# Performance work log

Hardware: AMD Instinct MI355X
Metric: run time of the kernel (lower is better)

Reference implementation:

```python
import jax, jax.numpy as jnp
import numpy as np
from jax import lax

BITS = 8  # w_p = a_p = 8 (HAWQ int8)

def _round_ste(x):
    # straight-through round (quant-aware training semantics)
    return x + lax.stop_gradient(jnp.round(x) - x)

def _quant_act(x):
    # QuantAct: symmetric per-tensor activation fake-quant; returns (quantized x, scale)
    n = 2.0 ** (BITS - 1) - 1.0
    sf = jnp.maximum(jnp.max(jnp.abs(x)) / n, 1e-8)
    q = jnp.clip(_round_ste(x / sf), -n, n)
    return q * sf, sf

def _quant_conv(x, w, b, pre_sf, stride, pad):
    # QuantConv2d: per-output-channel symmetric weight quant, integer conv on
    # x/pre_sf with rounded weights, rescale by pre_sf * w_sf. Bias quantized at
    # combined scale. Returns (float output, w_sf) for scale propagation.
    n = 2.0 ** (BITS - 1) - 1.0
    w_sf = jnp.maximum(jnp.max(jnp.abs(w), axis=(1, 2, 3)) / n, 1e-8)
    w_int = _round_ste(w / w_sf[:, None, None, None])
    b_sf = w_sf * pre_sf
    b_int = _round_ste(b / b_sf)
    y = lax.conv_general_dilated(x / pre_sf, w_int, (stride, stride),
                                 [(pad, pad), (pad, pad)],
                                 dimension_numbers=('NCHW', 'OIHW', 'NCHW'))
    return (y + b_int[None, :, None, None]) * b_sf[None, :, None, None], w_sf

def _bn(x, g, b, m, v, eps=1e-5):
    # BatchNorm2d in eval mode (running stats), folded into scale/shift
    inv = g / jnp.sqrt(v + eps)
    return x * inv[None, :, None, None] + (b - m * inv)[None, :, None, None]

def _quant_linear(x, w, b, pre_sf):
    # QuantLinear: per-output-row symmetric weight quant
    n = 2.0 ** (BITS - 1) - 1.0
    w_sf = jnp.maximum(jnp.max(jnp.abs(w), axis=1) / n, 1e-8)
    w_int = _round_ste(w / w_sf[:, None])
    b_sf = w_sf * pre_sf
    b_int = _round_ste(b / b_sf)
    return ((x / pre_sf) @ w_int.T + b_int[None, :]) * b_sf[None, :]

def _forward(x, w0, b0, g0, bb0, m0, v0, w1, b1, g1, bb1, m1, v1,
             w2, b2, g2, bb2, m2, v2, w3, b3, g3, bb3, m3, v3,
             w4, b4, g4, bb4, m4, v4, wd, bd):
    x, psf = _quant_act(x)
    x, _ = _quant_conv(x, w0, b0, psf, 1, 1)   # [B,32,32,32]
    x = _bn(x, g0, bb0, m0, v0)
    x, psf = _quant_act(x)
    x, _ = _quant_conv(x, w1, b1, psf, 1, 0)   # 1x1 -> [B,4,32,32]
    x = _bn(x, g1, bb1, m1, v1)
    x, psf = _quant_act(x)
    x, _ = _quant_conv(x, w2, b2, psf, 2, 1)   # [B,32,16,16]
    x = _bn(x, g2, bb2, m2, v2)
    x, psf = _quant_act(x)
    x, _ = _quant_conv(x, w3, b3, psf, 2, 1)   # [B,32,8,8]
    x = _bn(x, g3, bb3, m3, v3)
    x, psf = _quant_act(x)
    x, _ = _quant_conv(x, w4, b4, psf, 1, 1)   # [B,32,8,8]
    x = _bn(x, g4, bb4, m4, v4)
    x, psf = _quant_act(x)
    x = x.reshape(-1, 2048)                    # 32*8*8 = 2048
    x = _quant_linear(x, wd, bd, psf)          # [B,10]
    return jax.nn.softmax(x, axis=0)           # dim=0 as in original module

def setup_inputs() -> dict:
    key = jax.random.key(0)
    ks = jax.random.split(key, 40)
    B = 1024
    inp = {"x": jax.random.normal(ks[0], (B, 3, 32, 32), jnp.float32)}
    conv_shapes = [(32, 3, 3, 3), (4, 32, 1, 1), (32, 4, 3, 3), (32, 32, 3, 3), (32, 32, 3, 3)]
    for i, s in enumerate(conv_shapes):
        c = s[0]
        inp[f"w{i}"] = jax.random.normal(ks[1 + i], s, jnp.float32) * 0.1
        inp[f"b{i}"] = jax.random.normal(ks[6 + i], (c,), jnp.float32) * 0.01
        inp[f"g{i}"] = 1.0 + 0.1 * jax.random.normal(ks[11 + i], (c,), jnp.float32)
        inp[f"bb{i}"] = 0.1 * jax.random.normal(ks[16 + i], (c,), jnp.float32)
        inp[f"m{i}"] = 0.1 * jax.random.normal(ks[21 + i], (c,), jnp.float32)
        inp[f"v{i}"] = 0.5 + jax.random.uniform(ks[26 + i], (c,), jnp.float32)
    inp["wd"] = jax.random.normal(ks[31], (10, 2048), jnp.float32) * 0.05
    inp["bd"] = jnp.zeros((10,), jnp.float32)
    return inp

def reference(x, w0, b0, g0, bb0, m0, v0, w1, b1, g1, bb1, m1, v1,
              w2, b2, g2, bb2, m2, v2, w3, b3, g3, bb3, m3, v3,
              w4, b4, g4, bb4, m4, v4, wd, bd):
    return _forward(x, w0, b0, g0, bb0, m0, v0, w1, b1, g1, bb1, m1, v1,
                    w2, b2, g2, bb2, m2, v2, w3, b3, g3, bb3, m3, v3,
                    w4, b4, g4, bb4, m4, v4, wd, bd)
```

## Files before the change

### kernel.cpp

```cpp
#include <hip/hip_runtime.h>

#define DI __device__ __forceinline__

constexpr int OFF_WSF0 = 384;
constexpr int OFF_BNS0 = 416;
constexpr int OFF_BNB0 = 448;
constexpr int OFF_W0I  = 480;
constexpr int OFF_WSF1 = 1344;
constexpr int OFF_BNS1 = 1348;
constexpr int OFF_BNB1 = 1352;
constexpr int OFF_W1I  = 1356;
constexpr int OFF_WSF2 = 1484;
constexpr int OFF_BNS2 = 1516;
constexpr int OFF_BNB2 = 1548;
constexpr int OFF_W2I  = 1580;
constexpr int OFF_WSF3 = 2732;
constexpr int OFF_BNS3 = 2764;
constexpr int OFF_BNB3 = 2796;
constexpr int OFF_W3I  = 2828;
constexpr int OFF_WSF4 = 12044;
constexpr int OFF_BNS4 = 12076;
constexpr int OFF_BNB4 = 12108;
constexpr int OFF_W4I  = 12140;
constexpr int OFF_WSFD = 21356;
constexpr int OFF_WDI  = 21368;
constexpr int OFF_LOG  = 41856;
constexpr int OFF_ACT  = 52224;
constexpr long ACT_A_OFF = OFF_ACT;
constexpr long ACT_B_OFF = OFF_ACT + 8388608L;

DI float quantv(float x, float sf) {
    float q = rintf(x / sf);
    return fminf(fmaxf(q, -127.0f), 127.0f);
}
DI float get_sf(const unsigned* umax, int slot) {
    const unsigned* p = umax + slot * 64;
    unsigned m = 0u;
    #pragma unroll
    for (int i = 0; i < 64; ++i) m = m > p[i] ? m : p[i];
    return fmaxf(__uint_as_float(m) / 127.0f, 1e-8f);
}
DI void block_max_atomic(float v, unsigned* dst) {
    __shared__ float redm_[4];
    #pragma unroll
    for (int o = 32; o; o >>= 1) v = fmaxf(v, __shfl_down(v, o, 64));
    int wid = threadIdx.x >> 6;
    if ((threadIdx.x & 63) == 0) redm_[wid] = v;
    __syncthreads();
    if (threadIdx.x == 0) {
        int nw = blockDim.x >> 6;
        float m = redm_[0];
        for (int i = 1; i < nw; ++i) m = fmaxf(m, redm_[i]);
        atomicMax(dst + (blockIdx.x & 63), __float_as_uint(m));
    }
}

struct PrepEntry {
    const float *w, *g, *bb, *m, *v;
    float *wsf, *wint, *bns, *bnb;
    int K; int has_bn;
};
struct PrepAll { PrepEntry e[6]; unsigned* umax; };

__global__ __launch_bounds__(256) void k_prep_all(PrepAll pa) {
    int blk = blockIdx.x;
    if (blk == 142) {
        for (int i = threadIdx.x; i < 384; i += 256) pa.umax[i] = 0u;
        return;
    }
    int layer, oc;
    if      (blk < 32)  { layer = 0; oc = blk; }
    else if (blk < 36)  { layer = 1; oc = blk - 32; }
    else if (blk < 68)  { layer = 2; oc = blk - 36; }
    else if (blk < 100) { layer = 3; oc = blk - 68; }
    else if (blk < 132) { layer = 4; oc = blk - 100; }
    else                { layer = 5; oc = blk - 132; }
    PrepEntry a = pa.e[layer];
    const float* wr = a.w + (long)oc * a.K;
    float mx = 0.f;
    for (int i = threadIdx.x; i < a.K; i += 256) mx = fmaxf(mx, fabsf(wr[i]));
    __shared__ float red[4];
    __shared__ float s_sf;
    #pragma unroll
    for (int o = 32; o; o >>= 1) mx = fmaxf(mx, __shfl_down(mx, o, 64));
    if ((threadIdx.x & 63) == 0) red[threadIdx.x >> 6] = mx;
    __syncthreads();
    if (threadIdx.x == 0) {
        float t = fmaxf(fmaxf(red[0], red[1]), fmaxf(red[2], red[3]));
        t = fmaxf(t / 127.0f, 1e-8f);
        a.wsf[oc] = t; s_sf = t;
        if (a.has_bn) {
            float inv = a.g[oc] / sqrtf(a.v[oc] + 1e-5f);
            a.bns[oc] = inv;
            a.bnb[oc] = a.bb[oc] - a.m[oc] * inv;
        }
    }
    __syncthreads();
    float sf = s_sf;
    for (int i = threadIdx.x; i < a.K; i += 256) a.wint[(long)oc * a.K + i] = rintf(wr[i] / sf);
}

__global__ __launch_bounds__(256) void k_absmax(const float4* __restrict__ x, int n4, unsigned* dst) {
    float m = 0.f;
    for (int i = blockIdx.x * blockDim.x + threadIdx.x; i < n4; i += gridDim.x * blockDim.x) {
        float4 t = x[i];
        m = fmaxf(m, fmaxf(fmaxf(fabsf(t.x), fabsf(t.y)), fmaxf(fabsf(t.z), fabsf(t.w))));
    }
    block_max_atomic(m, dst);
}

__global__ __launch_bounds__(256) void k_conv0maxN(
    const float* __restrict__ x, const float* __restrict__ w0i,
    const float* __restrict__ wsf0, const float* __restrict__ bias0,
    const float* __restrict__ bns0, const float* __restrict__ bnb0,
    const unsigned* __restrict__ umax, unsigned* __restrict__ mout) {
    __shared__ float tile[3 * 18 * 36];
    __shared__ float wlds[27 * 32];
    __shared__ float As[32], Cs[32];
    const int b  = blockIdx.x >> 1;
    const int r0 = (blockIdx.x & 1) * 16;
    const int tid = threadIdx.x;
    const float sfx = get_sf(umax, 0);
    if (tid < 32) {
        int oc = tid;
        float bsf = wsf0[oc] * sfx;
        float bint = rintf(bias0[oc] / bsf);
        float a = bsf * bns0[oc];
        As[oc] = a;
        Cs[oc] = fmaf(bint, a, bnb0[oc]);
    }
    for (int i = tid; i < 1944; i += 256) tile[i] = 0.f;
    for (int i = tid; i < 864; i += 256) {
        int k = i >> 5, oc = i & 31;
        wlds[i] = w0i[oc * 27 + k];
    }
    __syncthreads();
    const float* xb = x + (long)b * 3072;
    for (int i = tid; i < 1728; i += 256) {
        int ci = i / 576, rem = i - ci * 576;
        int rr = rem >> 5, cc = rem & 31;
        int gr = r0 - 1 + rr;
        if ((unsigned)gr < 32u)
            tile[ci * 648 + rr * 36 + cc + 1] = quantv(xb[ci * 1024 + gr * 32 + cc], sfx);
    }
    __syncthreads();
    const int oc0  = (tid >> 5) * 4;
    const int pxg  = tid & 31;
    const int row  = pxg >> 1;
    const int wcol = (pxg & 1) * 16;
    float acc[4][16];
    #pragma unroll
    for (int o = 0; o < 4; ++o)
        #pragma unroll
        for (int p = 0; p < 16; ++p) acc[o][p] = 0.f;
    #pragma unroll 1
    for (int kk = 0; kk < 9; ++kk) {
        int ci = kk / 3, ky = kk - ci * 3;
        const float* rp = tile + ci * 648 + (row + ky) * 36 + wcol;
        float wn[20];
        #pragma unroll
        for (int d = 0; d < 5; ++d) *(float4*)&wn[4 * d] = *(const float4*)&rp[4 * d];
        #pragma unroll
        for (int kx = 0; kx < 3; ++kx) {
            float4 wv = *(const float4*)&wlds[(kk * 3 + kx) * 32 + oc0];
            const float* wf = &wv.x;
            #pragma unroll
            for (int o = 0; o < 4; ++o)
                #pragma unroll
                for (int p = 0; p < 16; ++p)
                    acc[o][p] = fmaf(wn[p + kx], wf[o], acc[o][p]);
        }
    }
    float lmax = 0.f;
    #pragma unroll
    for (int o = 0; o < 4; ++o) {
        float A = As[oc0 + o], C = Cs[oc0 + o];
        #pragma unroll
        for (int p = 0; p < 16; ++p)
            lmax = fmaxf(lmax, fabsf(fmaf(acc[o][p], A, C)));
    }
    block_max_atomic(lmax, mout);
}

__global__ __launch_bounds__(256) void k_conv01n(
    const float* __restrict__ x, const float* __restrict__ w0i,
    const float* __restrict__ wsf0, const float* __restrict__ bias0,
    const float* __restrict__ bns0, const float* __restrict__ bnb0,
    const float* __restrict__ w1i,
    const float* __restrict__ wsf1, const float* __restrict__ bias1,
    const float* __restrict__ bns1, const float* __restrict__ bnb1,
    const unsigned* __restrict__ umax, unsigned* __restrict__ mout,
    float* __restrict__ out) {
    __shared__ float tile[2 * 3672];
    __shared__ float wls0[896];
    __shared__ float wls1[128];
    __shared__ float As[32], Cs[32];
    __shared__ float A1s[4], C1s[4];
    const int tid = threadIdx.x;
    const long b2 = (long)blockIdx.x * 2;
    const float sfx = get_sf(umax, 0);
    const float sf1 = get_sf(umax, 1);
    if (tid < 32) {
        int oc = tid;
        float bsf = wsf0[oc] * sfx;
        float bint = rintf(bias0[oc] / bsf);
        float a = bsf * bns0[oc];
        As[oc] = a;
        Cs[oc] = fmaf(bint, a, bnb0[oc]);
    }
    if (tid >= 64 && tid < 68) {
        int oc = tid - 64;
        float bsf = wsf1[oc] * sf1;
        float bint = rintf(bias1[oc] / bsf);
        float a = bsf * bns1[oc];
        A1s[oc] = a;
        C1s[oc] = fmaf(bint, a, bnb1[oc]);
    }
    for (int i = tid; i < 2 * 3672; i += 256) tile[i] = 0.f;
    for (int i = tid; i < 864; i += 256) {
        int oc = i / 27, k = i - oc * 27;
        wls0[oc * 28 + k] = w0i[i];
    }
    if (tid < 128) {
        int o1 = tid >> 5, oc = tid & 31;
        wls1[oc * 4 + o1] = w1i[tid];
    }
    __syncthreads();
    for (int i = tid; i < 6144; i += 256) {
        int img = i / 3072, rem = i - img * 3072;
        int ci = rem >> 10, px = rem & 1023;
        int iy = px >> 5, ix = px & 31;
        tile[img * 3672 + ci * 1224 + (iy + 1) * 36 + (ix + 1)] =
            quantv(x[(b2 + img) * 3072 + rem], sfx);
    }
    __syncthreads();
    const int img = tid >> 7;
    const int pt  = tid & 127;
    const int h   = pt >> 2;
    const int w0  = (pt & 3) * 8;
    float win[3][3][12];
    #pragma unroll
    for (int ci = 0; ci < 3; ++ci)
        #pragma unroll
        for (int ky = 0; ky < 3; ++ky) {
            const float* rp = tile + img * 3672 + ci * 1224 + (h + ky) * 36 + w0;
            #pragma unroll
            for (int d = 0; d < 3; ++d)
                *(float4*)&win[ci][ky][4 * d] = *(const float4*)&rp[4 * d];
        }
    float acc1[4][8];
    #pragma unroll
    for (int o = 0; o < 4; ++o)
        #pragma unroll
        for (int p = 0; p < 8; ++p) acc1[o][p] = 0.f;
    #pragma unroll 1
    for (int oc = 0; oc < 32; ++oc) {
        float wreg[28];
        const float4* wp4 = (const float4*)&wls0[oc * 28];
        #pragma unroll
        for (int d = 0; d < 7; ++d) *(float4*)&wreg[4 * d] = wp4[d];
        float acc0[8];
        #pragma unroll
        for (int p = 0; p < 8; ++p) acc0[p] = 0.f;
        #pragma unroll
        for (int ci = 0; ci < 3; ++ci)
            #pragma unroll
            for (int ky = 0; ky < 3; ++ky)
                #pragma unroll
                for (int kx = 0; kx < 3; ++kx) {
                    float wv = wreg[ci * 9 + ky * 3 + kx];
                    #pragma unroll
                    for (int p = 0; p < 8; ++p)
                        acc0[p] = fmaf(win[ci][ky][p + kx], wv, acc0[p]);
                }
        float A = As[oc], C = Cs[oc];
        float4 w1v = *(const float4*)&wls1[oc * 4];
        const float* w1f = &w1v.x;
        #pragma unroll
        for (int p = 0; p < 8; ++p) {
            float q = quantv(fmaf(acc0[p], A, C), sf1);
            #pragma unroll
            for (int o = 0; o < 4; ++o)
                acc1[o][p] = fmaf(q, w1f[o], acc1[o][p]);
        }
    }
    float lmax = 0.f;
    float* ob = out + (b2 + img) * 4096;
    #pragma unroll
    for (int o = 0; o < 4; ++o) {
        float A = A1s[o], C = C1s[o];
        float r[8];
        #pragma unroll
        for (int p = 0; p < 8; ++p) {
            float y = fmaf(acc1[o][p], A, C);
            r[p] = y;
            lmax = fmaxf(lmax, fabsf(y));
        }
        *(float4*)&ob[o * 1024 + h * 32 + w0]     = *(float4*)&r[0];
        *(float4*)&ob[o * 1024 + h * 32 + w0 + 4] = *(float4*)&r[4];
    }
    block_max_atomic(lmax, mout);
}

__global__ __launch_bounds__(256) void k_conv2c(
    const float* __restrict__ inp, const float* __restrict__ wgl,
    const float* __restrict__ wsf, const float* __restrict__ bias,
    const float* __restrict__ bns, const float* __restrict__ bnb,
    const unsigned* __restrict__ umax, unsigned* __restrict__ mout,
    float* __restrict__ out) {
    __shared__ float tile[4 * 34 * 36];
    __shared__ float wlds[36 * 32];
    __shared__ float As[32], Cs[32];
    const int tid = threadIdx.x;
    const float sf = get_sf(umax, 2);
    if (tid < 32) {
        int oc = tid;
        float bsf = wsf[oc] * sf;
        float bint = rintf(bias[oc] / bsf);
        float a = bsf * bns[oc];
        As[oc] = a;
        Cs[oc] = fmaf(bint, a, bnb[oc]);
    }
    for (int i = tid; i < 4896; i += 256) tile[i] = 0.f;
    for (int i = tid; i < 1152; i += 256) {
        int k = i >> 5, oc = i & 31;
        wlds[i] = wgl[oc * 36 + k];
    }
    __syncthreads();
    const float* ib = inp + (long)blockIdx.x * 4096;
    for (int i = tid; i < 4096; i += 256) {
        int ci = i >> 10, px = i & 1023;
        int iy = px >> 5, ix = px & 31;
        tile[ci * 1224 + (iy + 1) * 36 + (ix + 1)] = quantv(ib[i], sf);
    }
    __syncthreads();
    const int oc0 = (tid >> 6) * 8;
    const int pxq = tid & 63;
    const int h = pxq >> 2, c = pxq & 3;
    float acc[8][4];
    #pragma unroll
    for (int k = 0; k < 8; ++k)
        #pragma unroll
        for (int p = 0; p < 4; ++p) acc[k][p] = 0.f;
    #pragma unroll 1
    for (int ci = 0; ci < 4; ++ci) {
        #pragma unroll
        for (int ky = 0; ky < 3; ++ky) {
            const float* rp = tile + ci * 1224 + (2 * h + ky) * 36 + 8 * c;
            float wn[12];
            #pragma unroll
            for (int d = 0; d < 3; ++d) *(float4*)&wn[4 * d] = *(const float4*)&rp[4 * d];
            #pragma unroll
            for (int kx = 0; kx < 3; ++kx) {
                const float* wp = &wlds[(ci * 9 + ky * 3 + kx) * 32 + oc0];
                float4 wa = *(const float4*)&wp[0];
                float4 wb = *(const float4*)&wp[4];
                float wf[8] = {wa.x, wa.y, wa.z, wa.w, wb.x, wb.y, wb.z, wb.w};
                #pragma unroll
                for (int k = 0; k < 8; ++k)
                    #pragma unroll
                    for (int p = 0; p < 4; ++p)
                        acc[k][p] = fmaf(wn[2 * p + kx], wf[k], acc[k][p]);
            }
        }
    }
    float lmax = 0.f;
    float* ob = out + (long)blockIdx.x * 8192;
    #pragma unroll
    for (int k = 0; k < 8; ++k) {
        int oc = oc0 + k;
        float A = As[oc], C = Cs[oc];
        float4 r;
        float* rp = &r.x;
        #pragma unroll
        for (int p = 0; p < 4; ++p) {
            float y = fmaf(acc[k][p], A, C);
            rp[p] = y;
            lmax = fmaxf(lmax, fabsf(y));
        }
        *(float4*)&ob[oc * 256 + h * 16 + c * 4] = r;
    }
    block_max_atomic(lmax, mout);
}

template<int HIN, int S>
__global__ __launch_bounds__(256) void k_conv34b(
    const float* __restrict__ inp, const float* __restrict__ wi,
    const float* __restrict__ wsf, const float* __restrict__ bias,
    const float* __restrict__ bns, const float* __restrict__ bnb,
    const unsigned* __restrict__ umax, int slot, unsigned* __restrict__ mout,
    float* __restrict__ out) {
    constexpr int ROWS = HIN + 2;
    constexpr int RS   = (S == 2) ? 20 : 12;
    constexpr int TI   = 8 * ROWS * RS;
    constexpr int PIX  = HIN * HIN;
    constexpr int NELT = 2 * 8 * PIX;
    constexpr int WINW = (S == 2) ? 12 : 8;
    constexpr int ND   = (S == 2) ? 3 : 2;
    __shared__ float tile[2 * TI];
    __shared__ float wlds[72 * 36];
    __shared__ float As[32], Cs[32];
    const int tid  = threadIdx.x;
    const int imgl = tid >> 7;
    const int ocg  = (tid >> 4) & 7;
    const int pxq  = tid & 15;
    const int h = pxq >> 1, c = pxq & 1;
    const float sf = get_sf(umax, slot);
    if (tid < 32) {
        int oc = tid;
        float bsf = wsf[oc] * sf;
        float bint = rintf(bias[oc] / bsf);
        float a = bsf * bns[oc];
        As[oc] = a;
        Cs[oc] = fmaf(bint, a, bnb[oc]);
    }
    for (int i = tid; i < 2 * TI; i += 256) tile[i] = 0.f;
    float acc[16];
    #pragma unroll
    for (int i = 0; i < 16; ++i) acc[i] = 0.f;
    const float* ib = inp + (long)blockIdx.x * 2 * 32 * PIX;
    for (int ph = 0; ph < 4; ++ph) {
        __syncthreads();
        for (int i = tid; i < NELT; i += 256) {
            int im = i / (8 * PIX);
            int r  = i % (8 * PIX);
            int ci = r / PIX;
            int px = r % PIX;
            int iy = px / HIN, ix = px % HIN;
            tile[(im * 8 + ci) * (ROWS * RS) + (iy + 1) * RS + (ix + 1)] =
                quantv(ib[(long)(im * 32 + ph * 8 + ci) * PIX + px], sf);
        }
        for (int i = tid; i < 2304; i += 256) {
            int oc = i / 72, k = i - oc * 72;
            wlds[k * 36 + oc] = wi[oc * 288 + ph * 72 + k];
        }
        __syncthreads();
        const float* tb = tile + imgl * TI;
        #pragma unroll 2
        for (int ci = 0; ci < 8; ++ci) {
            float win[3][WINW];
            #pragma unroll
            for (int ky = 0; ky < 3; ++ky) {
                const float* rp = tb + ci * (ROWS * RS) + (S * h + ky) * RS + S * 4 * c;
                #pragma unroll
                for (int d = 0; d < ND; ++d)
                    *(float4*)&win[ky][4 * d] = *(const float4*)&rp[4 * d];
            }
            #pragma unroll
            for (int ky = 0; ky < 3; ++ky)
                #pragma unroll
                for (int kx = 0; kx < 3; ++kx) {
                    int j = ky * 3 + kx;
                    float4 wv = *(const float4*)&wlds[(ci * 9 + j) * 36 + ocg * 4];
                    float wvf[4] = {wv.x, wv.y, wv.z, wv.w};
                    #pragma unroll
                    for (int k = 0; k < 4; ++k)
                        #pragma unroll
                        for (int px = 0; px < 4; ++px)
                            acc[k * 4 + px] = fmaf(win[ky][S * px + kx], wvf[k], acc[k * 4 + px]);
                }
        }
    }
    float lmax = 0.f;
    long imgg = (long)blockIdx.x * 2 + imgl;
    #pragma unroll
    for (int k = 0; k < 4; ++k) {
        int oc = ocg * 4 + k;
        float A = As[oc], C = Cs[oc];
        float4 r;
        float* rp = &r.x;
        #pragma unroll
        for (int px = 0; px < 4; ++px) {
            float y = fmaf(acc[k * 4 + px], A, C);
            rp[px] = y;
            lmax = fmaxf(lmax, fabsf(y));
        }
        *(float4*)&out[(imgg * 32 + oc) * 64 + h * 8 + c * 4] = r;
    }
    block_max_atomic(lmax, mout);
}

__global__ __launch_bounds__(256) void k_fc(
    const float* __restrict__ act, const float* __restrict__ wdi,
    const float* __restrict__ wsfd, const float* __restrict__ bd,
    const unsigned* __restrict__ umax, float* __restrict__ logits) {
    int b = blockIdx.x;
    float sf = get_sf(umax, 5);
    const float* ab = act + (long)b * 2048;
    float acc[10];
    #pragma unroll
    for (int c = 0; c < 10; ++c) acc[c] = 0.f;
    #pragma unroll
    for (int k = 0; k < 8; ++k) {
        int j = threadIdx.x + 256 * k;
        float q = quantv(ab[j], sf);
        #pragma unroll
        for (int c = 0; c < 10; ++c) acc[c] = fmaf(q, wdi[c * 2048 + j], acc[c]);
    }
    #pragma unroll
    for (int c = 0; c < 10; ++c)
        #pragma unroll
        for (int o = 32; o; o >>= 1) acc[c] += __shfl_down(acc[c], o, 64);
    __shared__ float red[4][10];
    int wid = threadIdx.x >> 6;
    if ((threadIdx.x & 63) == 0)
        #pragma unroll
        for (int c = 0; c < 10; ++c) red[wid][c] = acc[c];
    __syncthreads();
    if (threadIdx.x < 10) {
        int c = threadIdx.x;
        float s = red[0][c] + red[1][c] + red[2][c] + red[3][c];
        float bsf = wsfd[c] * sf;
        float bint = rintf(bd[c] / bsf);
        logits[b * 10 + c] = (s + bint) * bsf;
    }
}

__global__ __launch_bounds__(256) void k_softmax(const float* __restrict__ logits, float* __restrict__ out) {
    int c = blockIdx.x;
    float v0 = logits[(threadIdx.x +   0) * 10 + c];
    float v1 = logits[(threadIdx.x + 256) * 10 + c];
    float v2 = logits[(threadIdx.x + 512) * 10 + c];
    float v3 = logits[(threadIdx.x + 768) * 10 + c];
    float mx = fmaxf(fmaxf(v0, v1), fmaxf(v2, v3));
    __shared__ float redm[4];
    __shared__ float reds[4];
    #pragma unroll
    for (int o = 32; o; o >>= 1) mx = fmaxf(mx, __shfl_down(mx, o, 64));
    if ((threadIdx.x & 63) == 0) redm[threadIdx.x >> 6] = mx;
    __syncthreads();
    mx = fmaxf(fmaxf(redm[0], redm[1]), fmaxf(redm[2], redm[3]));
    float e0 = expf(v0 - mx), e1 = expf(v1 - mx), e2 = expf(v2 - mx), e3 = expf(v3 - mx);
    float s = (e0 + e1) + (e2 + e3);
    #pragma unroll
    for (int o = 32; o; o >>= 1) s += __shfl_down(s, o, 64);
    if ((threadIdx.x & 63) == 0) reds[threadIdx.x >> 6] = s;
    __syncthreads();
    s = reds[0] + reds[1] + reds[2] + reds[3];
    out[(threadIdx.x +   0) * 10 + c] = e0 / s;
    out[(threadIdx.x + 256) * 10 + c] = e1 / s;
    out[(threadIdx.x + 512) * 10 + c] = e2 / s;
    out[(threadIdx.x + 768) * 10 + c] = e3 / s;
}

extern "C" void kernel_launch(void* const* d_in, const int* in_sizes, int n_in,
                              void* d_out, int out_size, void* d_ws, size_t ws_size,
                              hipStream_t stream) {
    (void)in_sizes; (void)n_in; (void)out_size; (void)ws_size;
    const float* x = (const float*)d_in[0];
    const float *w[5], *bia[5], *g[5], *bb[5], *m[5], *v[5];
    for (int i = 0; i < 5; ++i) {
        w[i]   = (const float*)d_in[1 + 6 * i + 0];
        bia[i] = (const float*)d_in[1 + 6 * i + 1];
        g[i]   = (const float*)d_in[1 + 6 * i + 2];
        bb[i]  = (const float*)d_in[1 + 6 * i + 3];
        m[i]   = (const float*)d_in[1 + 6 * i + 4];
        v[i]   = (const float*)d_in[1 + 6 * i + 5];
    }
    const float* wd = (const float*)d_in[31];
    const float* bd = (const float*)d_in[32];
    float* ws = (float*)d_ws;
    unsigned* umax = (unsigned*)ws;
    float* out = (float*)d_out;

    float* wsf0 = ws + OFF_WSF0; float* bns0 = ws + OFF_BNS0; float* bnb0 = ws + OFF_BNB0; float* w0i = ws + OFF_W0I;
    float* wsf1 = ws + OFF_WSF1; float* bns1 = ws + OFF_BNS1; float* bnb1 = ws + OFF_BNB1; float* w1i = ws + OFF_W1I;
    float* wsf2 = ws + OFF_WSF2; float* bns2 = ws + OFF_BNS2; float* bnb2 = ws + OFF_BNB2; float* w2i = ws + OFF_W2I;
    float* wsf3 = ws + OFF_WSF3; float* bns3 = ws + OFF_BNS3; float* bnb3 = ws + OFF_BNB3; float* w3i = ws + OFF_W3I;
    float* wsf4 = ws + OFF_WSF4; float* bns4 = ws + OFF_BNS4; float* bnb4 = ws + OFF_BNB4; float* w4i = ws + OFF_W4I;
    float* wsfd = ws + OFF_WSFD; float* wdi = ws + OFF_WDI;
    float* logits = ws + OFF_LOG;
    float* actA = ws + ACT_A_OFF;
    float* actB = ws + ACT_B_OFF;

    PrepAll pa;
    pa.umax = umax;
    const float* ww[6] = {w[0], w[1], w[2], w[3], w[4], wd};
    float* wsfp[6] = {wsf0, wsf1, wsf2, wsf3, wsf4, wsfd};
    float* wip[6]  = {w0i, w1i, w2i, w3i, w4i, wdi};
    float* bnsp[6] = {bns0, bns1, bns2, bns3, bns4, nullptr};
    float* bnbp[6] = {bnb0, bnb1, bnb2, bnb3, bnb4, nullptr};
    int Ks[6] = {27, 32, 36, 288, 288, 2048};
    for (int i = 0; i < 6; ++i) {
        pa.e[i].w = ww[i];
        pa.e[i].g = (i < 5) ? g[i] : nullptr;
        pa.e[i].bb = (i < 5) ? bb[i] : nullptr;
        pa.e[i].m = (i < 5) ? m[i] : nullptr;
        pa.e[i].v = (i < 5) ? v[i] : nullptr;
        pa.e[i].wsf = wsfp[i];
        pa.e[i].wint = wip[i];
        pa.e[i].bns = bnsp[i];
        pa.e[i].bnb = bnbp[i];
        pa.e[i].K = Ks[i];
        pa.e[i].has_bn = (i < 5) ? 1 : 0;
    }

    hipLaunchKernelGGL(k_prep_all, dim3(143), dim3(256), 0, stream, pa);
    hipLaunchKernelGGL(k_absmax, dim3(256), dim3(256), 0, stream,
                       (const float4*)x, 1024 * 3 * 32 * 32 / 4, umax + 0 * 64);
    hipLaunchKernelGGL(k_conv0maxN, dim3(2048), dim3(256), 0, stream,
                       x, w0i, wsf0, bia[0], bns0, bnb0, umax, umax + 1 * 64);
    hipLaunchKernelGGL(k_conv01n, dim3(512), dim3(256), 0, stream,
                       x, w0i, wsf0, bia[0], bns0, bnb0,
                       w1i, wsf1, bia[1], bns1, bnb1, umax, umax + 2 * 64, actB);
    hipLaunchKernelGGL(k_conv2c, dim3(1024), dim3(256), 0, stream,
                       actB, w2i, wsf2, bia[2], bns2, bnb2, umax, umax + 3 * 64, actA);
    hipLaunchKernelGGL((k_conv34b<16, 2>), dim3(512), dim3(256), 0, stream,
                       actA, w3i, wsf3, bia[3], bns3, bnb3, umax, 3, umax + 4 * 64, actB);
    hipLaunchKernelGGL((k_conv34b<8, 1>),  dim3(512), dim3(256), 0, stream,
                       actB, w4i, wsf4, bia[4], bns4, bnb4, umax, 4, umax + 5 * 64, actA);
    hipLaunchKernelGGL(k_fc, dim3(1024), dim3(256), 0, stream, actA, wdi, wsfd, bd, umax, logits);
    hipLaunchKernelGGL(k_softmax, dim3(10), dim3(256), 0, stream, logits, out);
}
```

Baseline: 192.9 us.

## Split fused conv0+conv1 kernel into half-image blocks with 2 pixels per thread

The fused conv0/1x1-conv1 kernel now has each block handle 16 rows of one image instead of two full images, and each thread computes 2 output pixels instead of 8. This quadruples the grid and cuts shared memory and registers per block, aiming for better occupancy and latency hiding across the GPU. In exchange, each block reloads its 3x3 weights and recomputes its halo rows, and per-thread reuse of the input window and weights drops. The absmax kernel grid is also raised from 256 to 1024 blocks.

```diff
diff --git a/kernel.cpp b/kernel.cpp
--- a/kernel.cpp
+++ b/kernel.cpp
@@ -191,13 +191,14 @@
     const float* __restrict__ bns1, const float* __restrict__ bnb1,
     const unsigned* __restrict__ umax, unsigned* __restrict__ mout,
     float* __restrict__ out) {
-    __shared__ float tile[2 * 3672];
+    __shared__ float tile[1944];
     __shared__ float wls0[896];
     __shared__ float wls1[128];
     __shared__ float As[32], Cs[32];
     __shared__ float A1s[4], C1s[4];
+    const int b  = blockIdx.x >> 1;
+    const int r0 = (blockIdx.x & 1) * 16;
     const int tid = threadIdx.x;
-    const long b2 = (long)blockIdx.x * 2;
     const float sfx = get_sf(umax, 0);
     const float sf1 = get_sf(umax, 1);
     if (tid < 32) {
@@ -216,52 +217,46 @@
         A1s[oc] = a;
         C1s[oc] = fmaf(bint, a, bnb1[oc]);
     }
-    for (int i = tid; i < 2 * 3672; i += 256) tile[i] = 0.f;
+    for (int i = tid; i < 1944; i += 256) tile[i] = 0.f;
     for (int i = tid; i < 864; i += 256) {
         int oc = i / 27, k = i - oc * 27;
         wls0[oc * 28 + k] = w0i[i];
     }
-    if (tid < 128) {
-        int o1 = tid >> 5, oc = tid & 31;
-        wls1[oc * 4 + o1] = w1i[tid];
-    }
-    __syncthreads();
-    for (int i = tid; i < 6144; i += 256) {
-        int img = i / 3072, rem = i - img * 3072;
-        int ci = rem >> 10, px = rem & 1023;
-        int iy = px >> 5, ix = px & 31;
-        tile[img * 3672 + ci * 1224 + (iy + 1) * 36 + (ix + 1)] =
-            quantv(x[(b2 + img) * 3072 + rem], sfx);
-    }
-    __syncthreads();
-    const int img = tid >> 7;
-    const int pt  = tid & 127;
-    const int h   = pt >> 2;
-    const int w0  = (pt & 3) * 8;
-    float win[3][3][12];
+    if (tid >= 128 && tid < 256) {
+        int j = tid - 128;
+        wls1[(j & 31) * 4 + (j >> 5)] = w1i[j];
+    }
+    __syncthreads();
+    const float* xb = x + (long)b * 3072;
+    for (int i = tid; i < 1728; i += 256) {
+        int ci = i / 576, rem = i - ci * 576;
+        int rr = rem >> 5, cc = rem & 31;
+        int gr = r0 - 1 + rr;
+        if ((unsigned)gr < 32u)
+            tile[ci * 648 + rr * 36 + cc + 1] = quantv(xb[ci * 1024 + gr * 32 + cc], sfx);
+    }
+    __syncthreads();
+    const int h   = tid >> 4;
+    const int w0c = (tid & 15) * 2;
+    float win[3][3][4];
     #pragma unroll
     for (int ci = 0; ci < 3; ++ci)
         #pragma unroll
         for (int ky = 0; ky < 3; ++ky) {
-            const float* rp = tile + img * 3672 + ci * 1224 + (h + ky) * 36 + w0;
+            const int base = ci * 648 + (h + ky) * 36 + w0c;
             #pragma unroll
-            for (int d = 0; d < 3; ++d)
-                *(float4*)&win[ci][ky][4 * d] = *(const float4*)&rp[4 * d];
-        }
-    float acc1[4][8];
-    #pragma unroll
-    for (int o = 0; o < 4; ++o)
-        #pragma unroll
-        for (int p = 0; p < 8; ++p) acc1[o][p] = 0.f;
+            for (int d = 0; d < 4; ++d) win[ci][ky][d] = tile[base + d];
+        }
+    float acc1[4][2];
+    #pragma unroll
+    for (int o = 0; o < 4; ++o) { acc1[o][0] = 0.f; acc1[o][1] = 0.f; }
     #pragma unroll 1
     for (int oc = 0; oc < 32; ++oc) {
         float wreg[28];
         const float4* wp4 = (const float4*)&wls0[oc * 28];
         #pragma unroll
         for (int d = 0; d < 7; ++d) *(float4*)&wreg[4 * d] = wp4[d];
-        float acc0[8];
-        #pragma unroll
-        for (int p = 0; p < 8; ++p) acc0[p] = 0.f;
+        float a0 = 0.f, a1 = 0.f;
         #pragma unroll
         for (int ci = 0; ci < 3; ++ci)
             #pragma unroll
@@ -269,35 +264,27 @@
                 #pragma unroll
                 for (int kx = 0; kx < 3; ++kx) {
                     float wv = wreg[ci * 9 + ky * 3 + kx];
-                    #pragma unroll
-                    for (int p = 0; p < 8; ++p)
-                        acc0[p] = fmaf(win[ci][ky][p + kx], wv, acc0[p]);
+                    a0 = fmaf(win[ci][ky][kx],     wv, a0);
+                    a1 = fmaf(win[ci][ky][kx + 1], wv, a1);
                 }
         float A = As[oc], C = Cs[oc];
-        float4 w1v = *(const float4*)&wls1[oc * 4];
-        const float* w1f = &w1v.x;
-        #pragma unroll
-        for (int p = 0; p < 8; ++p) {
-            float q = quantv(fmaf(acc0[p], A, C), sf1);
-            #pragma unroll
-            for (int o = 0; o < 4; ++o)
-                acc1[o][p] = fmaf(q, w1f[o], acc1[o][p]);
-        }
+        float q0 = quantv(fmaf(a0, A, C), sf1);
+        float q1 = quantv(fmaf(a1, A, C), sf1);
+        const float4 w1v = *(const float4*)&wls1[oc * 4];
+        acc1[0][0] = fmaf(q0, w1v.x, acc1[0][0]); acc1[0][1] = fmaf(q1, w1v.x, acc1[0][1]);
+        acc1[1][0] = fmaf(q0, w1v.y, acc1[1][0]); acc1[1][1] = fmaf(q1, w1v.y, acc1[1][1]);
+        acc1[2][0] = fmaf(q0, w1v.z, acc1[2][0]); acc1[2][1] = fmaf(q1, w1v.z, acc1[2][1]);
+        acc1[3][0] = fmaf(q0, w1v.w, acc1[3][0]); acc1[3][1] = fmaf(q1, w1v.w, acc1[3][1]);
     }
     float lmax = 0.f;
-    float* ob = out + (b2 + img) * 4096;
+    float* ob = out + (long)b * 4096 + (r0 + h) * 32 + w0c;
     #pragma unroll
     for (int o = 0; o < 4; ++o) {
-        float A = A1s[o], C = C1s[o];
-        float r[8];
-        #pragma unroll
-        for (int p = 0; p < 8; ++p) {
-            float y = fmaf(acc1[o][p], A, C);
-            r[p] = y;
-            lmax = fmaxf(lmax, fabsf(y));
-        }
-        *(float4*)&ob[o * 1024 + h * 32 + w0]     = *(float4*)&r[0];
-        *(float4*)&ob[o * 1024 + h * 32 + w0 + 4] = *(float4*)&r[4];
+        float y0 = fmaf(acc1[o][0], A1s[o], C1s[o]);
+        float y1 = fmaf(acc1[o][1], A1s[o], C1s[o]);
+        lmax = fmaxf(lmax, fmaxf(fabsf(y0), fabsf(y1)));
+        float2 r2; r2.x = y0; r2.y = y1;
+        *(float2*)&ob[o * 1024] = r2;
     }
     block_max_atomic(lmax, mout);
 }
@@ -596,11 +583,11 @@
     }
 
     hipLaunchKernelGGL(k_prep_all, dim3(143), dim3(256), 0, stream, pa);
-    hipLaunchKernelGGL(k_absmax, dim3(256), dim3(256), 0, stream,
+    hipLaunchKernelGGL(k_absmax, dim3(1024), dim3(256), 0, stream,
                        (const float4*)x, 1024 * 3 * 32 * 32 / 4, umax + 0 * 64);
     hipLaunchKernelGGL(k_conv0maxN, dim3(2048), dim3(256), 0, stream,
                        x, w0i, wsf0, bia[0], bns0, bnb0, umax, umax + 1 * 64);
-    hipLaunchKernelGGL(k_conv01n, dim3(512), dim3(256), 0, stream,
+    hipLaunchKernelGGL(k_conv01n, dim3(2048), dim3(256), 0, stream,
                        x, w0i, wsf0, bia[0], bns0, bnb0,
                        w1i, wsf1, bia[1], bns1, bnb1, umax, umax + 2 * 64, actB);
     hipLaunchKernelGGL(k_conv2c, dim3(1024), dim3(256), 0, stream,
```

Result: faster. 185.2 us (-4.0%).
